# Optimization experiments

Measured on AMD Instinct MI355X. Metric: run time of the kernel, lower is better.

Reference implementation:

```python
import jax, jax.numpy as jnp
import numpy as np

N, E, DIM, HID, TEMB = 50000, 600000, 128, 128, 8
IN_DIM = 3 * DIM + TEMB  # zi, zj, |zi-zj|, type_emb


def setup_inputs() -> dict:
    key = jax.random.key(0)
    ks = jax.random.split(key, 16)
    s = lambda *sh: 1.0 / np.sqrt(sh[-1])
    return {
        "z": jax.random.normal(ks[0], (N, DIM), jnp.float32),
        "edge_index": jax.random.randint(ks[1], (2, E), 0, N, jnp.int64),
        "edge_type": jax.random.randint(ks[2], (E,), 0, 2, jnp.int64),
        "type_emb": jax.random.normal(ks[3], (2, TEMB), jnp.float32),
        "ew1": jax.random.normal(ks[4], (HID, IN_DIM), jnp.float32) * s(HID, IN_DIM),
        "eb1": jnp.zeros((HID,), jnp.float32),
        "ew2": jax.random.normal(ks[5], (1, HID), jnp.float32) * s(1, HID),
        "eb2": jnp.zeros((1,), jnp.float32),
        "mw1": jax.random.normal(ks[6], (DIM, DIM), jnp.float32) * s(DIM, DIM),
        "mb1": jnp.zeros((DIM,), jnp.float32),
        "mw2": jax.random.normal(ks[7], (DIM, DIM), jnp.float32) * s(DIM, DIM),
        "mb2": jnp.zeros((DIM,), jnp.float32),
        "gamma": jnp.ones((DIM,), jnp.float32),
        "beta": jnp.zeros((DIM,), jnp.float32),
    }


def reference(z, edge_index, edge_type, type_emb, ew1, eb1, ew2, eb2,
              mw1, mb1, mw2, mb2, gamma, beta):
    src, dst = edge_index[0], edge_index[1]
    zi = z[src]          # [E, DIM]
    zj = z[dst]          # [E, DIM]
    te = type_emb[edge_type]  # [E, TEMB]
    e_in = jnp.concatenate([zi, zj, jnp.abs(zi - zj), te], axis=1)  # [E, IN_DIM]

    # edge MLP -> scalar weight per edge, sigmoid squashed
    h = jax.nn.relu(e_in @ ew1.T + eb1)
    w = jax.nn.sigmoid((h @ ew2.T + eb2)[:, 0])  # [E]

    n = z.shape[0]
    # numerically-stable segment softmax over edges grouped by src
    max_per_src = jnp.full((n,), -1e9, dtype=z.dtype).at[src].max(w)
    w_exp = jnp.exp(w - max_per_src[src])
    sum_per_src = jax.ops.segment_sum(w_exp, src, num_segments=n)
    alpha = w_exp / (sum_per_src[src] + 1e-12)  # [E]

    # message MLP on destination features, weighted by alpha
    msg = (jax.nn.relu(zj @ mw1.T + mb1) @ mw2.T + mb2) * alpha[:, None]  # [E, DIM]
    agg = jax.ops.segment_sum(msg, src, num_segments=n)  # [N, DIM]

    # residual + LayerNorm (dropout is identity in eval mode)
    x = z + agg
    mu = jnp.mean(x, axis=-1, keepdims=True)
    var = jnp.mean(jnp.square(x - mu), axis=-1, keepdims=True)
    out = (x - mu) * jax.lax.rsqrt(var + 1e-5) * gamma + beta
    return (out, alpha)
```

## Files before the change

### kernel.cpp

```cpp
#include <hip/hip_runtime.h>
#include <math.h>

constexpr int NN  = 50000;
constexpr int NE  = 600000;
constexpr int D   = 128;
constexpr int IND = 392;

typedef __attribute__((ext_vector_type(8))) short bf16x8;
typedef __attribute__((ext_vector_type(4))) float f32x4;

__device__ __forceinline__ float4 ld4(const float* p) { return *reinterpret_cast<const float4*>(p); }

__device__ __forceinline__ unsigned short f2bf(float f) {
  unsigned int u = __float_as_uint(f);
  u += 0x7fffu + ((u >> 16) & 1u);
  return (unsigned short)(u >> 16);
}
__device__ __forceinline__ float bf2f(unsigned short s) {
  return __uint_as_float(((unsigned int)s) << 16);
}

__global__ __launch_bounds__(256) void k_prep(
    const float* __restrict__ ew1, const float* __restrict__ type_emb,
    const float* __restrict__ mw1, const float* __restrict__ mw2,
    unsigned short* __restrict__ Wab, unsigned short* __restrict__ Wbb,
    unsigned short* __restrict__ Wcb,
    unsigned short* __restrict__ m1h, unsigned short* __restrict__ m1l,
    unsigned short* __restrict__ m2h, unsigned short* __restrict__ m2l,
    float* __restrict__ tvg)
{
  int g = blockIdx.x * 256 + threadIdx.x;
  int o = g >> 7, k = g & 127;
  Wab[g] = f2bf(ew1[o * IND + k]);
  Wbb[g] = f2bf(ew1[o * IND + 128 + k]);
  Wcb[g] = f2bf(ew1[o * IND + 256 + k]);
  float w1 = mw1[g];
  unsigned short h1 = f2bf(w1);
  m1h[g] = h1; m1l[g] = f2bf(w1 - bf2f(h1));
  float w2 = mw2[g];
  unsigned short h2 = f2bf(w2);
  m2h[g] = h2; m2l[g] = f2bf(w2 - bf2f(h2));
  if (blockIdx.x == 0) {
    int t = threadIdx.x, oo = t & 127, ty = t >> 7;
    float s = 0.f;
#pragma unroll
    for (int j = 0; j < 8; ++j) s += ew1[oo * IND + 384 + j] * type_emb[ty * 8 + j];
    tvg[ty * 128 + oo] = s;
  }
}

template <int TERMS>
__device__ __forceinline__ void mm_acc(
    const unsigned short (*Xh)[136], const unsigned short (*Xl)[136],
    const unsigned short (*Wh)[136], const unsigned short (*Wl)[136],
    int me, int r, int q, f32x4 acc[8])
{
#pragma unroll
  for (int ks = 0; ks < 4; ++ks) {
    bf16x8 ah = *reinterpret_cast<const bf16x8*>(&Xh[me + r][ks * 32 + q * 8]);
    bf16x8 al;
    if (TERMS >= 2) al = *reinterpret_cast<const bf16x8*>(&Xl[me + r][ks * 32 + q * 8]);
#pragma unroll
    for (int nt = 0; nt < 8; ++nt) {
      bf16x8 bh = *reinterpret_cast<const bf16x8*>(&Wh[nt * 16 + r][ks * 32 + q * 8]);
      acc[nt] = __builtin_amdgcn_mfma_f32_16x16x32_bf16(ah, bh, acc[nt], 0, 0, 0);
      if (TERMS >= 2)
        acc[nt] = __builtin_amdgcn_mfma_f32_16x16x32_bf16(al, bh, acc[nt], 0, 0, 0);
      if (TERMS == 3) {
        bf16x8 bl = *reinterpret_cast<const bf16x8*>(&Wl[nt * 16 + r][ks * 32 + q * 8]);
        acc[nt] = __builtin_amdgcn_mfma_f32_16x16x32_bf16(ah, bl, acc[nt], 0, 0, 0);
      }
    }
  }
}

__global__ __launch_bounds__(512, 1) void k_node_mfma(
    const float* __restrict__ z,
    const unsigned short* __restrict__ Wab, const unsigned short* __restrict__ Wbb,
    const unsigned short* __restrict__ m1h, const unsigned short* __restrict__ m1l,
    const unsigned short* __restrict__ m2h, const unsigned short* __restrict__ m2l,
    const float* __restrict__ mb1, const float* __restrict__ mb2,
    unsigned short* __restrict__ Ab, unsigned short* __restrict__ Bb,
    unsigned short* __restrict__ Mb, unsigned short* __restrict__ zb)
{
  __shared__ unsigned short Xh[128][136], Xl[128][136];
  __shared__ unsigned short Wh[128][136], Wl[128][136];
  const int t  = threadIdx.x;
  const int n0 = blockIdx.x * 128;

#pragma unroll
  for (int it = 0; it < 8; ++it) {
    int f = it * 512 + t, rr = f >> 5, c4 = (f & 31) * 4;
    int n = n0 + rr; if (n >= NN) n = NN - 1;
    float4 v = ld4(&z[(size_t)n * D + c4]);
    ushort4 hi, lo;
    hi.x = f2bf(v.x); lo.x = f2bf(v.x - bf2f(hi.x));
    hi.y = f2bf(v.y); lo.y = f2bf(v.y - bf2f(hi.y));
    hi.z = f2bf(v.z); lo.z = f2bf(v.z - bf2f(hi.z));
    hi.w = f2bf(v.w); lo.w = f2bf(v.w - bf2f(hi.w));
    *reinterpret_cast<ushort4*>(&Xh[rr][c4]) = hi;
    *reinterpret_cast<ushort4*>(&Xl[rr][c4]) = lo;
    if (n0 + rr < NN)
      *reinterpret_cast<ushort4*>(&zb[(size_t)(n0 + rr) * D + c4]) = hi;
  }
#pragma unroll
  for (int it = 0; it < 4; ++it) {
    int f = it * 512 + t, row = f >> 4, c8 = (f & 15) * 8;
    *reinterpret_cast<bf16x8*>(&Wh[row][c8]) =
        *reinterpret_cast<const bf16x8*>(&Wab[row * 128 + c8]);
  }
  __syncthreads();

  const int l = t & 63, q = l >> 4, r = l & 15;
  const int me = (t >> 6) * 16;

  f32x4 acc[8];

#pragma unroll
  for (int nt = 0; nt < 8; ++nt) acc[nt] = (f32x4){0.f, 0.f, 0.f, 0.f};
  mm_acc<1>(Xh, Xl, Wh, Wl, me, r, q, acc);
#pragma unroll
  for (int nt = 0; nt < 8; ++nt)
#pragma unroll
    for (int i = 0; i < 4; ++i) {
      int n = n0 + me + q * 4 + i;
      if (n < NN) Ab[(size_t)n * D + nt * 16 + r] = f2bf(acc[nt][i]);
    }
  __syncthreads();

#pragma unroll
  for (int it = 0; it < 4; ++it) {
    int f = it * 512 + t, row = f >> 4, c8 = (f & 15) * 8;
    *reinterpret_cast<bf16x8*>(&Wh[row][c8]) =
        *reinterpret_cast<const bf16x8*>(&Wbb[row * 128 + c8]);
  }
  __syncthreads();
#pragma unroll
  for (int nt = 0; nt < 8; ++nt) acc[nt] = (f32x4){0.f, 0.f, 0.f, 0.f};
  mm_acc<1>(Xh, Xl, Wh, Wl, me, r, q, acc);
#pragma unroll
  for (int nt = 0; nt < 8; ++nt)
#pragma unroll
    for (int i = 0; i < 4; ++i) {
      int n = n0 + me + q * 4 + i;
      if (n < NN) Bb[(size_t)n * D + nt * 16 + r] = f2bf(acc[nt][i]);
    }
  __syncthreads();

#pragma unroll
  for (int it = 0; it < 4; ++it) {
    int f = it * 512 + t, row = f >> 4, c8 = (f & 15) * 8;
    *reinterpret_cast<bf16x8*>(&Wh[row][c8]) =
        *reinterpret_cast<const bf16x8*>(&m1h[row * 128 + c8]);
    *reinterpret_cast<bf16x8*>(&Wl[row][c8]) =
        *reinterpret_cast<const bf16x8*>(&m1l[row * 128 + c8]);
  }
  __syncthreads();
#pragma unroll
  for (int nt = 0; nt < 8; ++nt) acc[nt] = (f32x4){0.f, 0.f, 0.f, 0.f};
  mm_acc<3>(Xh, Xl, Wh, Wl, me, r, q, acc);
#pragma unroll
  for (int nt = 0; nt < 8; ++nt) {
    int col = nt * 16 + r;
    float b1 = mb1[col];
#pragma unroll
    for (int i = 0; i < 4; ++i) {
      float h = fmaxf(acc[nt][i] + b1, 0.0f);
      unsigned short hh = f2bf(h);
      Xh[me + q * 4 + i][col] = hh;
      Xl[me + q * 4 + i][col] = f2bf(h - bf2f(hh));
    }
  }
  __syncthreads();

#pragma unroll
  for (int it = 0; it < 4; ++it) {
    int f = it * 512 + t, row = f >> 4, c8 = (f & 15) * 8;
    *reinterpret_cast<bf16x8*>(&Wh[row][c8]) =
        *reinterpret_cast<const bf16x8*>(&m2h[row * 128 + c8]);
    *reinterpret_cast<bf16x8*>(&Wl[row][c8]) =
        *reinterpret_cast<const bf16x8*>(&m2l[row * 128 + c8]);
  }
  __syncthreads();
#pragma unroll
  for (int nt = 0; nt < 8; ++nt) acc[nt] = (f32x4){0.f, 0.f, 0.f, 0.f};
  mm_acc<3>(Xh, Xl, Wh, Wl, me, r, q, acc);
#pragma unroll
  for (int nt = 0; nt < 8; ++nt) {
    int col = nt * 16 + r;
    float b2 = mb2[col];
#pragma unroll
    for (int i = 0; i < 4; ++i) {
      int n = n0 + me + q * 4 + i;
      if (n < NN) Mb[(size_t)n * D + col] = f2bf(acc[nt][i] + b2);
    }
  }
}

constexpr int SNB = 196;

__global__ __launch_bounds__(256) void k_hist(const int* __restrict__ ei,
                                              int* __restrict__ deg)
{
  int e = blockIdx.x * 256 + threadIdx.x;
  if (e < NE) atomicAdd(&deg[ei[e]], 1);
}

__global__ __launch_bounds__(256) void k_scan1(const int* __restrict__ deg,
                                               int* __restrict__ pre,
                                               int* __restrict__ bsum)
{
  __shared__ int ps[256];
  const int t = threadIdx.x, b = blockIdx.x;
  const int i = b * 256 + t;
  int v = (i < NN) ? deg[i] : 0;
  ps[t] = v;
  __syncthreads();
  for (int off = 1; off < 256; off <<= 1) {
    int u = (t >= off) ? ps[t - off] : 0;
    __syncthreads();
    ps[t] += u;
    __syncthreads();
  }
  pre[i] = ps[t] - v;
  if (t == 255) bsum[b] = ps[255];
}

__global__ __launch_bounds__(256) void k_scan2(const int* __restrict__ bsum,
                                               int* __restrict__ bbase)
{
  __shared__ int ps[256];
  const int t = threadIdx.x;
  int v = (t < SNB) ? bsum[t] : 0;
  ps[t] = v;
  __syncthreads();
  for (int off = 1; off < 256; off <<= 1) {
    int u = (t >= off) ? ps[t - off] : 0;
    __syncthreads();
    ps[t] += u;
    __syncthreads();
  }
  if (t < SNB) bbase[t] = ps[t] - v;
}

__global__ __launch_bounds__(256) void k_scan3(const int* __restrict__ pre,
                                               const int* __restrict__ bbase,
                                               int* __restrict__ rowptr,
                                               int* __restrict__ cursor)
{
  const int t = threadIdx.x, b = blockIdx.x;
  const int i = b * 256 + t;
  if (i < NN) {
    int v = pre[i] + bbase[b];
    rowptr[i] = v;
    cursor[i] = v;
  }
  if (i == 0) rowptr[NN] = NE;
}

__global__ __launch_bounds__(256) void k_fill(const int* __restrict__ ei,
                                              int* __restrict__ cursor,
                                              int* __restrict__ eid,
                                              int* __restrict__ de_perm)
{
  int e = blockIdx.x * 256 + threadIdx.x;
  if (e < NE) {
    int pos = atomicAdd(&cursor[ei[e]], 1);
    eid[pos] = e;
    de_perm[pos] = ei[NE + e];
  }
}

__global__ __launch_bounds__(512, 6) void k_edge_mfma(
    const unsigned short* __restrict__ zb, const int* __restrict__ ei,
    const int* __restrict__ etype,
    const unsigned short* __restrict__ Wcb, const float* __restrict__ tvg,
    const float* __restrict__ eb1, const float* __restrict__ ew2,
    const float* __restrict__ eb2,
    const unsigned short* __restrict__ Ab, const unsigned short* __restrict__ Bb,
    const int* __restrict__ eid, const int* __restrict__ de_perm,
    float* __restrict__ wexp_perm)
{
  __shared__ unsigned short Xb[128 * 128];
  __shared__ unsigned short Wb[64 * 128];
  __shared__ unsigned short se[128], de[128];
  __shared__ unsigned char  tyg[128];

  const int t = threadIdx.x;
  const int nx = gridDim.x >> 3;
  const int sb = (blockIdx.x & 7) * nx + (blockIdx.x >> 3);
  const int e0 = sb * 128;

  if (t < 128) {
    int pos = e0 + t;
    if (pos < NE) {
      int e  = eid[pos];
      se[t]  = (unsigned short)ei[e];
      de[t]  = (unsigned short)de_perm[pos];
      tyg[t] = (unsigned char)etype[e];
    } else { se[t] = 0; de[t] = 0; tyg[t] = 0; }
  }
#pragma unroll
  for (int it = 0; it < 2; ++it) {
    int f = it * 512 + t, row = f >> 4, c = f & 15;
    int a = (row * 256 + c * 16) ^ ((row & 7) << 4);
    *reinterpret_cast<bf16x8*>((char*)Wb + a) =
        *reinterpret_cast<const bf16x8*>(&Wcb[row * 128 + c * 8]);
  }
  __syncthreads();

#pragma unroll
  for (int it = 0; it < 8; ++it) {
    int f = it * 512 + t, r = f >> 5, c4 = f & 31;
    ushort4 a4 = *reinterpret_cast<const ushort4*>(&zb[(size_t)se[r] * D + c4 * 4]);
    ushort4 b4 = *reinterpret_cast<const ushort4*>(&zb[(size_t)de[r] * D + c4 * 4]);
    ushort4 v;
    v.x = f2bf(fabsf(bf2f(a4.x) - bf2f(b4.x)));
    v.y = f2bf(fabsf(bf2f(a4.y) - bf2f(b4.y)));
    v.z = f2bf(fabsf(bf2f(a4.z) - bf2f(b4.z)));
    v.w = f2bf(fabsf(bf2f(a4.w) - bf2f(b4.w)));
    int a = (r * 256 + c4 * 8) ^ ((r & 7) << 4);
    *reinterpret_cast<ushort4*>((char*)Xb + a) = v;
  }
  __syncthreads();

  const int l = t & 63, q = l >> 4, r = l & 15;
  const int me = (t >> 6) * 16;

  f32x4 acc[8];
#pragma unroll
  for (int nt = 0; nt < 8; ++nt) acc[nt] = (f32x4){0.f, 0.f, 0.f, 0.f};

#pragma unroll
  for (int ks = 0; ks < 4; ++ks) {
    int xa = ((me + r) * 256 + ks * 64 + q * 16) ^ ((r & 7) << 4);
    bf16x8 a = *reinterpret_cast<const bf16x8*>((const char*)Xb + xa);
#pragma unroll
    for (int ntl = 0; ntl < 4; ++ntl) {
      int wrow = ntl * 16 + r;
      int wa = (wrow * 256 + ks * 64 + q * 16) ^ ((wrow & 7) << 4);
      bf16x8 b = *reinterpret_cast<const bf16x8*>((const char*)Wb + wa);
      acc[ntl] = __builtin_amdgcn_mfma_f32_16x16x32_bf16(a, b, acc[ntl], 0, 0, 0);
    }
  }
  __syncthreads();

#pragma unroll
  for (int it = 0; it < 2; ++it) {
    int f = it * 512 + t, row = f >> 4, c = f & 15;
    int a = (row * 256 + c * 16) ^ ((row & 7) << 4);
    *reinterpret_cast<bf16x8*>((char*)Wb + a) =
        *reinterpret_cast<const bf16x8*>(&Wcb[(64 + row) * 128 + c * 8]);
  }
  __syncthreads();

#pragma unroll
  for (int ks = 0; ks < 4; ++ks) {
    int xa = ((me + r) * 256 + ks * 64 + q * 16) ^ ((r & 7) << 4);
    bf16x8 a = *reinterpret_cast<const bf16x8*>((const char*)Xb + xa);
#pragma unroll
    for (int ntl = 0; ntl < 4; ++ntl) {
      int wrow = ntl * 16 + r;
      int wa = (wrow * 256 + ks * 64 + q * 16) ^ ((wrow & 7) << 4);
      bf16x8 b = *reinterpret_cast<const bf16x8*>((const char*)Wb + wa);
      acc[4 + ntl] = __builtin_amdgcn_mfma_f32_16x16x32_bf16(a, b, acc[4 + ntl], 0, 0, 0);
    }
  }

  int s[4], dd[4], ty[4];
#pragma unroll
  for (int i = 0; i < 4; ++i) {
    int el = me + q * 4 + i;
    s[i] = se[el]; dd[i] = de[el]; ty[i] = tyg[el];
  }
  float p[4] = {0.f, 0.f, 0.f, 0.f};
#pragma unroll
  for (int nt = 0; nt < 8; ++nt) {
    int col = nt * 16 + r;
    float e1  = eb1[col], w2 = ew2[col];
    float tva = tvg[col], tvb = tvg[128 + col];
#pragma unroll
    for (int i = 0; i < 4; ++i) {
      float h = acc[nt][i] + bf2f(Ab[(size_t)s[i] * D + col])
              + bf2f(Bb[(size_t)dd[i] * D + col]) + (ty[i] ? tvb : tva) + e1;
      p[i] += fmaxf(h, 0.f) * w2;
    }
  }
#pragma unroll
  for (int m = 1; m < 16; m <<= 1) {
#pragma unroll
    for (int i = 0; i < 4; ++i) p[i] += __shfl_xor(p[i], m);
  }
  if (r == 0) {
    float b2 = eb2[0];
#pragma unroll
    for (int i = 0; i < 4; ++i) {
      int pos = e0 + me + q * 4 + i;
      if (pos < NE) {
        float w = 1.0f / (1.0f + expf(-(p[i] + b2)));
        wexp_perm[pos] = expf(w);
      }
    }
  }
}

__global__ __launch_bounds__(256) void k_agg(
    const float* __restrict__ z, const float* __restrict__ wexp_perm,
    const unsigned short* __restrict__ Mb, const int* __restrict__ rowptr,
    const int* __restrict__ eid, const int* __restrict__ de_perm,
    const float* __restrict__ gamma, const float* __restrict__ beta,
    float* __restrict__ out, float* __restrict__ alpha_out)
{
  const int t = threadIdx.x;
  const int n = blockIdx.x * 4 + (t >> 6);
  const int l = t & 63;
  const int start = rowptr[n], end = rowptr[n + 1];

  float tot = 0.f;
  for (int base = start; base < end; base += 64) {
    if (base + l < end) tot += wexp_perm[base + l];
  }
#pragma unroll
  for (int off = 32; off; off >>= 1) tot += __shfl_xor(tot, off);
  const float inv = 1.0f / (tot + 1e-12f);

  float2 acc = make_float2(0.f, 0.f);
  for (int base = start; base < end; base += 64) {
    int cnt = min(64, end - base);
    int dd = 0;
    float al = 0.f;
    if (l < cnt) {
      int pos = base + l;
      al = wexp_perm[pos] * inv;
      dd = de_perm[pos];
      alpha_out[eid[pos]] = al;
    }
    for (int i = 0; i < cnt; ++i) {
      float a = __shfl(al, i);
      int   d = __shfl(dd, i);
      ushort2 m = *reinterpret_cast<const ushort2*>(&Mb[(size_t)d * D + l * 2]);
      acc.x = fmaf(a, bf2f(m.x), acc.x);
      acc.y = fmaf(a, bf2f(m.y), acc.y);
    }
  }

  float2 xz = *reinterpret_cast<const float2*>(&z[(size_t)n * D + l * 2]);
  float x0 = xz.x + acc.x, x1 = xz.y + acc.y;
  float s = x0 + x1;
#pragma unroll
  for (int off = 32; off; off >>= 1) s += __shfl_xor(s, off);
  const float mu = s * (1.0f / 128.0f);
  float d0 = x0 - mu, d1 = x1 - mu;
  float q = d0 * d0 + d1 * d1;
#pragma unroll
  for (int off = 32; off; off >>= 1) q += __shfl_xor(q, off);
  const float rstd = rsqrtf(q * (1.0f / 128.0f) + 1e-5f);
  float2 g = *reinterpret_cast<const float2*>(&gamma[l * 2]);
  float2 b = *reinterpret_cast<const float2*>(&beta[l * 2]);
  float2 o = make_float2(d0 * rstd * g.x + b.x, d1 * rstd * g.y + b.y);
  *reinterpret_cast<float2*>(&out[(size_t)n * D + l * 2]) = o;
}

extern "C" void kernel_launch(void* const* d_in, const int* in_sizes, int n_in,
                              void* d_out, int out_size, void* d_ws, size_t ws_size,
                              hipStream_t stream)
{
  const float* z        = (const float*)d_in[0];
  const int*   ei       = (const int*)d_in[1];
  const int*   etype    = (const int*)d_in[2];
  const float* type_emb = (const float*)d_in[3];
  const float* ew1      = (const float*)d_in[4];
  const float* eb1      = (const float*)d_in[5];
  const float* ew2      = (const float*)d_in[6];
  const float* eb2      = (const float*)d_in[7];
  const float* mw1      = (const float*)d_in[8];
  const float* mb1      = (const float*)d_in[9];
  const float* mw2      = (const float*)d_in[10];
  const float* mb2      = (const float*)d_in[11];
  const float* gamma    = (const float*)d_in[12];
  const float* beta     = (const float*)d_in[13];

  float*          ws        = (float*)d_ws;
  unsigned short* Ab        = (unsigned short*)(ws);
  unsigned short* Bb        = (unsigned short*)(ws + 3200000);
  unsigned short* Mb        = (unsigned short*)(ws + 6400000);
  unsigned short* zb        = (unsigned short*)(ws + 9600000);
  float*          wexp_perm = ws + 12800000;
  int*            deg       = (int*)(ws + 13400000);
  int*            rowptr    = deg + 50000;
  int*            cursor    = rowptr + 50004;
  int*            eid       = cursor + 50000;
  int*            de_perm   = eid + 600000;
  unsigned short* Wcb       = (unsigned short*)(ws + 14800000);
  float*          tvg       = ws + 14810000;
  unsigned short* Wab       = (unsigned short*)(ws + 14820000);
  unsigned short* Wbb       = (unsigned short*)(ws + 14830000);
  unsigned short* m1h       = (unsigned short*)(ws + 14840000);
  unsigned short* m1l       = (unsigned short*)(ws + 14850000);
  unsigned short* m2h       = (unsigned short*)(ws + 14860000);
  unsigned short* m2l       = (unsigned short*)(ws + 14870000);
  int*            pre       = (int*)(ws + 14880000);
  int*            bsum      = (int*)(ws + 14940000);
  int*            bbase     = (int*)(ws + 14941000);

  float* out       = (float*)d_out;
  float* alpha_out = out + (size_t)NN * D;

  hipMemsetAsync(deg, 0, 50000 * sizeof(int), stream);

  k_prep<<<64, 256, 0, stream>>>(ew1, type_emb, mw1, mw2,
                                 Wab, Wbb, Wcb, m1h, m1l, m2h, m2l, tvg);
  k_hist<<<(NE + 255) / 256, 256, 0, stream>>>(ei, deg);
  k_scan1<<<SNB, 256, 0, stream>>>(deg, pre, bsum);
  k_scan2<<<1, 256, 0, stream>>>(bsum, bbase);
  k_scan3<<<SNB, 256, 0, stream>>>(pre, bbase, rowptr, cursor);
  k_fill<<<(NE + 255) / 256, 256, 0, stream>>>(ei, cursor, eid, de_perm);
  k_node_mfma<<<(NN + 127) / 128, 512, 0, stream>>>(z, Wab, Wbb, m1h, m1l,
                                                    m2h, m2l, mb1, mb2,
                                                    Ab, Bb, Mb, zb);
  k_edge_mfma<<<(NE + 127) / 128, 512, 0, stream>>>(zb, ei, etype, Wcb, tvg,
                                                    eb1, ew2, eb2, Ab, Bb,
                                                    eid, de_perm, wexp_perm);
  k_agg<<<NN / 4, 256, 0, stream>>>(z, wexp_perm, Mb, rowptr, eid, de_perm,
                                    gamma, beta, out, alpha_out);
}
```

Baseline: 262.0 us.

## Compute zi/zj edge-MLP terms per edge instead of precomputing per-node projections

Moves the zi·Wa and zj·Wb products of the edge MLP from a per-node precompute (Ab/Bb tables) into the edge kernel, where each edge tile gathers zb rows for src and dst and runs three full 128-wide MFMA passes. This removes the two node-level GEMMs plus the scattered per-edge gathers of Ab/Bb rows in the epilogue. The cost is roughly three times the edge-level MFMA work and larger shared memory, so occupancy drops from 6 to 4 blocks per CU.

```diff
diff --git a/kernel.cpp b/kernel.cpp
--- a/kernel.cpp
+++ b/kernel.cpp
@@ -76,11 +76,9 @@
 
 __global__ __launch_bounds__(512, 1) void k_node_mfma(
     const float* __restrict__ z,
-    const unsigned short* __restrict__ Wab, const unsigned short* __restrict__ Wbb,
     const unsigned short* __restrict__ m1h, const unsigned short* __restrict__ m1l,
     const unsigned short* __restrict__ m2h, const unsigned short* __restrict__ m2l,
     const float* __restrict__ mb1, const float* __restrict__ mb2,
-    unsigned short* __restrict__ Ab, unsigned short* __restrict__ Bb,
     unsigned short* __restrict__ Mb, unsigned short* __restrict__ zb)
 {
   __shared__ unsigned short Xh[128][136], Xl[128][136];
@@ -107,55 +105,17 @@
   for (int it = 0; it < 4; ++it) {
     int f = it * 512 + t, row = f >> 4, c8 = (f & 15) * 8;
     *reinterpret_cast<bf16x8*>(&Wh[row][c8]) =
-        *reinterpret_cast<const bf16x8*>(&Wab[row * 128 + c8]);
-  }
-  __syncthreads();
-
-  const int l = t & 63, q = l >> 4, r = l & 15;
-  const int me = (t >> 6) * 16;
-
-  f32x4 acc[8];
-
-#pragma unroll
-  for (int nt = 0; nt < 8; ++nt) acc[nt] = (f32x4){0.f, 0.f, 0.f, 0.f};
-  mm_acc<1>(Xh, Xl, Wh, Wl, me, r, q, acc);
-#pragma unroll
-  for (int nt = 0; nt < 8; ++nt)
-#pragma unroll
-    for (int i = 0; i < 4; ++i) {
-      int n = n0 + me + q * 4 + i;
-      if (n < NN) Ab[(size_t)n * D + nt * 16 + r] = f2bf(acc[nt][i]);
-    }
-  __syncthreads();
-
-#pragma unroll
-  for (int it = 0; it < 4; ++it) {
-    int f = it * 512 + t, row = f >> 4, c8 = (f & 15) * 8;
-    *reinterpret_cast<bf16x8*>(&Wh[row][c8]) =
-        *reinterpret_cast<const bf16x8*>(&Wbb[row * 128 + c8]);
-  }
-  __syncthreads();
-#pragma unroll
-  for (int nt = 0; nt < 8; ++nt) acc[nt] = (f32x4){0.f, 0.f, 0.f, 0.f};
-  mm_acc<1>(Xh, Xl, Wh, Wl, me, r, q, acc);
-#pragma unroll
-  for (int nt = 0; nt < 8; ++nt)
-#pragma unroll
-    for (int i = 0; i < 4; ++i) {
-      int n = n0 + me + q * 4 + i;
-      if (n < NN) Bb[(size_t)n * D + nt * 16 + r] = f2bf(acc[nt][i]);
-    }
-  __syncthreads();
-
-#pragma unroll
-  for (int it = 0; it < 4; ++it) {
-    int f = it * 512 + t, row = f >> 4, c8 = (f & 15) * 8;
-    *reinterpret_cast<bf16x8*>(&Wh[row][c8]) =
         *reinterpret_cast<const bf16x8*>(&m1h[row * 128 + c8]);
     *reinterpret_cast<bf16x8*>(&Wl[row][c8]) =
         *reinterpret_cast<const bf16x8*>(&m1l[row * 128 + c8]);
   }
   __syncthreads();
+
+  const int l = t & 63, q = l >> 4, r = l & 15;
+  const int me = (t >> 6) * 16;
+
+  f32x4 acc[8];
+
 #pragma unroll
   for (int nt = 0; nt < 8; ++nt) acc[nt] = (f32x4){0.f, 0.f, 0.f, 0.f};
   mm_acc<3>(Xh, Xl, Wh, Wl, me, r, q, acc);
@@ -271,18 +231,17 @@
   }
 }
 
-__global__ __launch_bounds__(512, 6) void k_edge_mfma(
+__global__ __launch_bounds__(512, 4) void k_edge_mfma(
     const unsigned short* __restrict__ zb, const int* __restrict__ ei,
     const int* __restrict__ etype,
+    const unsigned short* __restrict__ Wab, const unsigned short* __restrict__ Wbb,
     const unsigned short* __restrict__ Wcb, const float* __restrict__ tvg,
     const float* __restrict__ eb1, const float* __restrict__ ew2,
     const float* __restrict__ eb2,
-    const unsigned short* __restrict__ Ab, const unsigned short* __restrict__ Bb,
     const int* __restrict__ eid, const int* __restrict__ de_perm,
     float* __restrict__ wexp_perm)
 {
-  __shared__ unsigned short Xb[128 * 128];
-  __shared__ unsigned short Wb[64 * 128];
+  __shared__ unsigned short S[32768];
   __shared__ unsigned short se[128], de[128];
   __shared__ unsigned char  tyg[128];
 
@@ -300,32 +259,47 @@
       tyg[t] = (unsigned char)etype[e];
     } else { se[t] = 0; de[t] = 0; tyg[t] = 0; }
   }
-#pragma unroll
-  for (int it = 0; it < 2; ++it) {
+  __syncthreads();
+
+#pragma unroll
+  for (int it = 0; it < 8; ++it) {
+    int f = it * 512 + t, r = f >> 5, c4 = f & 31;
+    int a = (r * 256 + c4 * 8) ^ ((r & 7) << 4);
+    ushort4 vi = *reinterpret_cast<const ushort4*>(&zb[(size_t)se[r] * D + c4 * 4]);
+    ushort4 vj = *reinterpret_cast<const ushort4*>(&zb[(size_t)de[r] * D + c4 * 4]);
+    *reinterpret_cast<ushort4*>((char*)S + a)         = vi;
+    *reinterpret_cast<ushort4*>((char*)S + 32768 + a) = vj;
+  }
+  __syncthreads();
+
+  const int l = t & 63, q = l >> 4, r = l & 15;
+  const int me = (t >> 6) * 16;
+
+  bf16x8 fi[4], fj[4], fd[4];
+#pragma unroll
+  for (int ks = 0; ks < 4; ++ks) {
+    int xa = ((me + r) * 256 + ks * 64 + q * 16) ^ ((r & 7) << 4);
+    fi[ks] = *reinterpret_cast<const bf16x8*>((const char*)S + xa);
+    fj[ks] = *reinterpret_cast<const bf16x8*>((const char*)S + 32768 + xa);
+#pragma unroll
+    for (int e = 0; e < 8; ++e) {
+      float ai = bf2f((unsigned short)fi[ks][e]);
+      float aj = bf2f((unsigned short)fj[ks][e]);
+      fd[ks][e] = (short)f2bf(fabsf(ai - aj));
+    }
+  }
+  __syncthreads();
+
+#pragma unroll
+  for (int it = 0; it < 4; ++it) {
     int f = it * 512 + t, row = f >> 4, c = f & 15;
     int a = (row * 256 + c * 16) ^ ((row & 7) << 4);
-    *reinterpret_cast<bf16x8*>((char*)Wb + a) =
-        *reinterpret_cast<const bf16x8*>(&Wcb[row * 128 + c * 8]);
-  }
-  __syncthreads();
-
-#pragma unroll
-  for (int it = 0; it < 8; ++it) {
-    int f = it * 512 + t, r = f >> 5, c4 = f & 31;
-    ushort4 a4 = *reinterpret_cast<const ushort4*>(&zb[(size_t)se[r] * D + c4 * 4]);
-    ushort4 b4 = *reinterpret_cast<const ushort4*>(&zb[(size_t)de[r] * D + c4 * 4]);
-    ushort4 v;
-    v.x = f2bf(fabsf(bf2f(a4.x) - bf2f(b4.x)));
-    v.y = f2bf(fabsf(bf2f(a4.y) - bf2f(b4.y)));
-    v.z = f2bf(fabsf(bf2f(a4.z) - bf2f(b4.z)));
-    v.w = f2bf(fabsf(bf2f(a4.w) - bf2f(b4.w)));
-    int a = (r * 256 + c4 * 8) ^ ((r & 7) << 4);
-    *reinterpret_cast<ushort4*>((char*)Xb + a) = v;
-  }
-  __syncthreads();
-
-  const int l = t & 63, q = l >> 4, r = l & 15;
-  const int me = (t >> 6) * 16;
+    *reinterpret_cast<bf16x8*>((char*)S + a) =
+        *reinterpret_cast<const bf16x8*>(&Wab[row * 128 + c * 8]);
+    *reinterpret_cast<bf16x8*>((char*)S + 32768 + a) =
+        *reinterpret_cast<const bf16x8*>(&Wbb[row * 128 + c * 8]);
+  }
+  __syncthreads();
 
   f32x4 acc[8];
 #pragma unroll
@@ -333,56 +307,50 @@
 
 #pragma unroll
   for (int ks = 0; ks < 4; ++ks) {
-    int xa = ((me + r) * 256 + ks * 64 + q * 16) ^ ((r & 7) << 4);
-    bf16x8 a = *reinterpret_cast<const bf16x8*>((const char*)Xb + xa);
-#pragma unroll
-    for (int ntl = 0; ntl < 4; ++ntl) {
-      int wrow = ntl * 16 + r;
+#pragma unroll
+    for (int nt = 0; nt < 8; ++nt) {
+      int wrow = nt * 16 + r;
       int wa = (wrow * 256 + ks * 64 + q * 16) ^ ((wrow & 7) << 4);
-      bf16x8 b = *reinterpret_cast<const bf16x8*>((const char*)Wb + wa);
-      acc[ntl] = __builtin_amdgcn_mfma_f32_16x16x32_bf16(a, b, acc[ntl], 0, 0, 0);
-    }
-  }
-  __syncthreads();
-
-#pragma unroll
-  for (int it = 0; it < 2; ++it) {
+      bf16x8 ba = *reinterpret_cast<const bf16x8*>((const char*)S + wa);
+      acc[nt] = __builtin_amdgcn_mfma_f32_16x16x32_bf16(fi[ks], ba, acc[nt], 0, 0, 0);
+      bf16x8 bb = *reinterpret_cast<const bf16x8*>((const char*)S + 32768 + wa);
+      acc[nt] = __builtin_amdgcn_mfma_f32_16x16x32_bf16(fj[ks], bb, acc[nt], 0, 0, 0);
+    }
+  }
+  __syncthreads();
+
+#pragma unroll
+  for (int it = 0; it < 4; ++it) {
     int f = it * 512 + t, row = f >> 4, c = f & 15;
     int a = (row * 256 + c * 16) ^ ((row & 7) << 4);
-    *reinterpret_cast<bf16x8*>((char*)Wb + a) =
-        *reinterpret_cast<const bf16x8*>(&Wcb[(64 + row) * 128 + c * 8]);
+    *reinterpret_cast<bf16x8*>((char*)S + a) =
+        *reinterpret_cast<const bf16x8*>(&Wcb[row * 128 + c * 8]);
   }
   __syncthreads();
 
 #pragma unroll
   for (int ks = 0; ks < 4; ++ks) {
-    int xa = ((me + r) * 256 + ks * 64 + q * 16) ^ ((r & 7) << 4);
-    bf16x8 a = *reinterpret_cast<const bf16x8*>((const char*)Xb + xa);
-#pragma unroll
-    for (int ntl = 0; ntl < 4; ++ntl) {
-      int wrow = ntl * 16 + r;
+#pragma unroll
+    for (int nt = 0; nt < 8; ++nt) {
+      int wrow = nt * 16 + r;
       int wa = (wrow * 256 + ks * 64 + q * 16) ^ ((wrow & 7) << 4);
-      bf16x8 b = *reinterpret_cast<const bf16x8*>((const char*)Wb + wa);
-      acc[4 + ntl] = __builtin_amdgcn_mfma_f32_16x16x32_bf16(a, b, acc[4 + ntl], 0, 0, 0);
-    }
-  }
-
-  int s[4], dd[4], ty[4];
-#pragma unroll
-  for (int i = 0; i < 4; ++i) {
-    int el = me + q * 4 + i;
-    s[i] = se[el]; dd[i] = de[el]; ty[i] = tyg[el];
-  }
+      bf16x8 bc = *reinterpret_cast<const bf16x8*>((const char*)S + wa);
+      acc[nt] = __builtin_amdgcn_mfma_f32_16x16x32_bf16(fd[ks], bc, acc[nt], 0, 0, 0);
+    }
+  }
+
+  int ty[4];
+#pragma unroll
+  for (int i = 0; i < 4; ++i) ty[i] = tyg[me + q * 4 + i];
   float p[4] = {0.f, 0.f, 0.f, 0.f};
 #pragma unroll
   for (int nt = 0; nt < 8; ++nt) {
     int col = nt * 16 + r;
     float e1  = eb1[col], w2 = ew2[col];
-    float tva = tvg[col], tvb = tvg[128 + col];
+    float tva = tvg[col] + e1, tvb = tvg[128 + col] + e1;
 #pragma unroll
     for (int i = 0; i < 4; ++i) {
-      float h = acc[nt][i] + bf2f(Ab[(size_t)s[i] * D + col])
-              + bf2f(Bb[(size_t)dd[i] * D + col]) + (ty[i] ? tvb : tva) + e1;
+      float h = acc[nt][i] + (ty[i] ? tvb : tva);
       p[i] += fmaxf(h, 0.f) * w2;
     }
   }
@@ -481,8 +449,6 @@
   const float* beta     = (const float*)d_in[13];
 
   float*          ws        = (float*)d_ws;
-  unsigned short* Ab        = (unsigned short*)(ws);
-  unsigned short* Bb        = (unsigned short*)(ws + 3200000);
   unsigned short* Mb        = (unsigned short*)(ws + 6400000);
   unsigned short* zb        = (unsigned short*)(ws + 9600000);
   float*          wexp_perm = ws + 12800000;
@@ -515,11 +481,10 @@
   k_scan2<<<1, 256, 0, stream>>>(bsum, bbase);
   k_scan3<<<SNB, 256, 0, stream>>>(pre, bbase, rowptr, cursor);
   k_fill<<<(NE + 255) / 256, 256, 0, stream>>>(ei, cursor, eid, de_perm);
-  k_node_mfma<<<(NN + 127) / 128, 512, 0, stream>>>(z, Wab, Wbb, m1h, m1l,
-                                                    m2h, m2l, mb1, mb2,
-                                                    Ab, Bb, Mb, zb);
-  k_edge_mfma<<<(NE + 127) / 128, 512, 0, stream>>>(zb, ei, etype, Wcb, tvg,
-                                                    eb1, ew2, eb2, Ab, Bb,
+  k_node_mfma<<<(NN + 127) / 128, 512, 0, stream>>>(z, m1h, m1l, m2h, m2l,
+                                                    mb1, mb2, Mb, zb);
+  k_edge_mfma<<<(NE + 127) / 128, 512, 0, stream>>>(zb, ei, etype, Wab, Wbb,
+                                                    Wcb, tvg, eb1, ew2, eb2,
                                                     eid, de_perm, wexp_perm);
   k_agg<<<NN / 4, 256, 0, stream>>>(z, wexp_perm, Mb, rowptr, eid, de_perm,
                                     gamma, beta, out, alpha_out);
```

Result: slower. 274.8 us (+4.9%).
